# Optimization experiments

Hardware: AMD Instinct MI355X
Metric: run time of the kernel (lower is better)

Reference implementation:

```python
import jax, jax.numpy as jnp
import numpy as np

B, NPG, DEG = 128, 400, 16
N, E = B * NPG, B * NPG * DEG
E_PER = E // B
K1, K2, K3 = 360, 324, 292  # ceil(0.9*400), ceil(0.9*360), ceil(0.9*324)
EPS = 1e-5


def setup_inputs() -> dict:
    key = jax.random.key(0)
    ks = jax.random.split(key, 48)
    # edges constrained within each graph (contiguous equal-size graphs)
    g = jnp.repeat(jnp.arange(B, dtype=jnp.int32), E_PER)
    src = jax.random.randint(ks[0], (E,), 0, NPG, dtype=jnp.int32) + g * NPG
    dst = jax.random.randint(ks[1], (E,), 0, NPG, dtype=jnp.int32) + g * NPG
    inp = {
        'x': jax.random.normal(ks[2], (N, 64), dtype=jnp.float32),
        'edge_index': jnp.stack([src, dst]),
        'batch': jnp.repeat(jnp.arange(B, dtype=jnp.int32), NPG),
    }
    def glorot(k, a, b):
        lim = float(np.sqrt(6.0 / (a + b)))
        return jax.random.uniform(k, (a, b), minval=-lim, maxval=lim, dtype=jnp.float32)
    conv_dims = [(64, 32), (32, 64), (64, 128), (128, 128)]
    for i, (a, b) in enumerate(conv_dims, 1):
        inp[f'W{i}'] = glorot(ks[2 + i], a, b)
        inp[f'b{i}'] = jnp.zeros((b,), jnp.float32)
    for i, d in zip((1, 2, 3), (32, 64, 128)):
        inp[f'p{i}'] = jax.random.uniform(ks[8 + i], (d,), minval=-1.0, maxval=1.0, dtype=jnp.float32) / float(np.sqrt(d))
    lin_dims = [(128, 64), (64, 64), (64, 32), (32, 16), (16, 1)]
    for i, (a, b) in enumerate(lin_dims, 1):
        inp[f'Lw{i}'] = glorot(ks[12 + i], a, b)
        inp[f'Lb{i}'] = jnp.zeros((b,), jnp.float32)
    for i, d in enumerate((64, 64, 32, 16), 1):
        inp[f'g{i}'] = jnp.ones((d,), jnp.float32)
        inp[f'be{i}'] = jnp.zeros((d,), jnp.float32)
    return inp


def _gcn(x, src, dst, emask, nmask, W, b):
    h = x @ W
    deg = nmask + jax.ops.segment_sum(emask, dst, num_segments=N)
    dinv = jnp.where(deg > 0, jax.lax.rsqrt(deg), 0.0)
    norm = dinv[src] * dinv[dst] * emask
    agg = jax.ops.segment_sum(h[src] * norm[:, None], dst, num_segments=N)
    agg = agg + h * (dinv * dinv * nmask)[:, None]  # self-loop term
    return (agg + b) * nmask[:, None]


def _topk_pool(x, nmask, p, k):
    # PyG TopKPooling: score = x.p/||p||, keep top-k per graph, x *= tanh(score)
    score = (x @ p) / jnp.linalg.norm(p)
    sel = jnp.where(nmask > 0, score, -jnp.inf).reshape(B, NPG)
    _, idx = jax.lax.top_k(sel, k)
    gidx = (idx + (jnp.arange(B) * NPG)[:, None]).reshape(-1)
    new_mask = jnp.zeros((N,), x.dtype).at[gidx].set(1.0)
    return x * (jnp.tanh(score) * new_mask)[:, None], new_mask


def reference(x, edge_index, batch, W1, b1, p1, W2, b2, p2, W3, b3, p3, W4, b4,
              Lw1, Lb1, Lw2, Lb2, Lw3, Lb3, Lw4, Lb4, Lw5, Lb5,
              g1, be1, g2, be2, g3, be3, g4, be4):
    src, dst = edge_index[0], edge_index[1]
    nmask = jnp.ones((N,), jnp.float32)
    emask = jnp.ones((E,), jnp.float32)
    x = jax.nn.relu(_gcn(x, src, dst, emask, nmask, W1, b1))
    x, nmask = _topk_pool(x, nmask, p1, K1)
    emask = emask * nmask[src] * nmask[dst]
    x = jax.nn.relu(_gcn(x, src, dst, emask, nmask, W2, b2))
    x, nmask = _topk_pool(x, nmask, p2, K2)
    emask = emask * nmask[src] * nmask[dst]
    x = jax.nn.relu(_gcn(x, src, dst, emask, nmask, W3, b3))
    x, nmask = _topk_pool(x, nmask, p3, K3)
    emask = emask * nmask[src] * nmask[dst]
    x = jax.nn.relu(_gcn(x, src, dst, emask, nmask, W4, b4))
    h = x.reshape(B, NPG, -1).max(axis=1)
    def lin_bn(h, W, bb, ga, be):
        h = h @ W + bb
        m = h.mean(0)
        v = h.var(0)  # biased, matches BatchNorm1d training normalization
        return jax.nn.relu(ga * (h - m) / jnp.sqrt(v + EPS) + be)
    h = lin_bn(h, Lw1, Lb1, g1, be1)
    h = lin_bn(h, Lw2, Lb2, g2, be2)
    h = lin_bn(h, Lw3, Lb3, g3, be3)
    h = lin_bn(h, Lw4, Lb4, g4, be4)
    return h @ Lw5 + Lb5
```

## Files before the change

kernel.cpp:

```cpp
#include <hip/hip_runtime.h>
#include <math.h>

#define NNODES 51200
#define BGRAPHS 128
#define NPG 400
#define NEDGES 819200
#define EPG 6400
#define SLP 7680

__global__ __launch_bounds__(512) void csr_build_kernel(
    const int* __restrict__ src, const int* __restrict__ dst,
    unsigned short* __restrict__ slg, int* __restrict__ gsg, int* __restrict__ gcg,
    float* __restrict__ nmask, float* __restrict__ dinv, float* __restrict__ sc,
    float* __restrict__ hp) {
    __shared__ int deg[NPG];
    __shared__ int incl[512];
    __shared__ int gs[NPG];
    __shared__ int cur[NPG];
    const int g = blockIdx.x, t = threadIdx.x;
    for (int i = t; i < NPG; i += 512) deg[i] = 0;
    if (t < 128) hp[g * 128 + t] = 0.0f;
    __syncthreads();
    for (int e = t; e < EPG; e += 512)
        atomicAdd(&deg[dst[g * EPG + e] - g * NPG], 1);
    __syncthreads();
    const int d = (t < NPG) ? deg[t] : 0;
    const int p = (d + 3) >> 2;
    incl[t] = p;
    __syncthreads();
    for (int off = 1; off < 512; off <<= 1) {
        int add = (t >= off) ? incl[t - off] : 0;
        __syncthreads();
        incl[t] += add;
        __syncthreads();
    }
    if (t < NPG) {
        const int gstart = incl[t] - p;
        gs[t] = gstart;
        gsg[g * NPG + t] = gstart;
        gcg[g * NPG + t] = p;
        cur[t] = gstart * 4;
        nmask[g * NPG + t] = 1.0f;
        const float dv = rsqrtf(1.0f + (float)d);
        dinv[g * NPG + t] = dv;
        sc[g * NPG + t] = dv;
    }
    __syncthreads();
    for (int e = t; e < EPG; e += 512) {
        int dl = dst[g * EPG + e] - g * NPG;
        int pos = atomicAdd(&cur[dl], 1);
        slg[g * SLP + pos] = (unsigned short)(src[g * EPG + e] - g * NPG);
    }
    __syncthreads();
    if (t < NPG) {
        const int end = (gs[t] + p) * 4;
        for (int i = cur[t]; i < end; i++) slg[g * SLP + i] = (unsigned short)NPG;
    }
}

template<int IN, int OUT, int MODE>
__global__ __launch_bounds__(256) void gemm_kernel(
    const float* __restrict__ X, const float* __restrict__ W,
    const float* __restrict__ bias, const float* __restrict__ nmask,
    float* __restrict__ H, const float* __restrict__ p,
    float* __restrict__ score, float* __restrict__ hp) {
    __shared__ __align__(16) float sX[64 * IN];
    __shared__ unsigned smax[256];
    const int row0 = blockIdx.x * 64;
    const int t = threadIdx.x;
    for (int i = t; i < 64 * IN / 4; i += 256)
        reinterpret_cast<float4*>(sX)[i] =
            reinterpret_cast<const float4*>(X + (size_t)row0 * IN)[i];
    if (MODE == 3) smax[t] = 0u;
    __syncthreads();
    constexpr int CG  = OUT / 4;
    constexpr int RG  = 256 / CG;
    constexpr int RPT = 64 / RG;
    const int c0 = (t % CG) * 4;
    const int r0 = (t / CG) * RPT;
    float acc[RPT][4];
#pragma unroll
    for (int r = 0; r < RPT; r++)
#pragma unroll
        for (int j = 0; j < 4; j++) acc[r][j] = 0.0f;
    for (int k4 = 0; k4 < IN / 4; k4++) {
        const float4 w0 = *reinterpret_cast<const float4*>(&W[(k4 * 4 + 0) * OUT + c0]);
        const float4 w1 = *reinterpret_cast<const float4*>(&W[(k4 * 4 + 1) * OUT + c0]);
        const float4 w2 = *reinterpret_cast<const float4*>(&W[(k4 * 4 + 2) * OUT + c0]);
        const float4 w3 = *reinterpret_cast<const float4*>(&W[(k4 * 4 + 3) * OUT + c0]);
#pragma unroll
        for (int r = 0; r < RPT; r++) {
            const float4 xv = *reinterpret_cast<const float4*>(&sX[(r0 + r) * IN + k4 * 4]);
            acc[r][0] += xv.x * w0.x + xv.y * w1.x + xv.z * w2.x + xv.w * w3.x;
            acc[r][1] += xv.x * w0.y + xv.y * w1.y + xv.z * w2.y + xv.w * w3.y;
            acc[r][2] += xv.x * w0.z + xv.y * w1.z + xv.z * w2.z + xv.w * w3.z;
            acc[r][3] += xv.x * w0.w + xv.y * w1.w + xv.z * w2.w + xv.w * w3.w;
        }
    }
    const int graph0 = row0 / 400;
    const int bnd = (graph0 + 1) * 400;
    float ps[RPT];
#pragma unroll
    for (int r = 0; r < RPT; r++) {
        const int row = row0 + r0 + r;
        float4 v = make_float4(acc[r][0], acc[r][1], acc[r][2], acc[r][3]);
        if (MODE >= 2) {
            const float4 b4 = *reinterpret_cast<const float4*>(&bias[c0]);
            const float m = nmask[row];
            v.x = fmaxf(v.x + b4.x, 0.0f) * m;
            v.y = fmaxf(v.y + b4.y, 0.0f) * m;
            v.z = fmaxf(v.z + b4.z, 0.0f) * m;
            v.w = fmaxf(v.w + b4.w, 0.0f) * m;
        }
        if (MODE != 3) *reinterpret_cast<float4*>(&H[(size_t)row * OUT + c0]) = v;
        if (MODE == 2) {
            const float4 p4 = *reinterpret_cast<const float4*>(&p[c0]);
            ps[r] = v.x * p4.x + v.y * p4.y + v.z * p4.z + v.w * p4.w;
        }
        if (MODE == 3) {
            const int seg = (row >= bnd) ? 1 : 0;
            const float mx = fmaxf(fmaxf(v.x, v.y), fmaxf(v.z, v.w));
            atomicMax(&smax[seg * 128 + c0 + 0], __float_as_uint(v.x));
            atomicMax(&smax[seg * 128 + c0 + 1], __float_as_uint(v.y));
            atomicMax(&smax[seg * 128 + c0 + 2], __float_as_uint(v.z));
            atomicMax(&smax[seg * 128 + c0 + 3], __float_as_uint(v.w));
            (void)mx;
        }
    }
    if (MODE == 2) {
#pragma unroll
        for (int r = 0; r < RPT; r++) {
#pragma unroll
            for (int off = 1; off < CG; off <<= 1) ps[r] += __shfl_xor(ps[r], off);
        }
        if ((t % CG) == 0) {
#pragma unroll
            for (int r = 0; r < RPT; r++) score[row0 + r0 + r] = ps[r];
        }
    }
    if (MODE == 3) {
        __syncthreads();
        unsigned* hpu = reinterpret_cast<unsigned*>(hp);
        if (t < 128) atomicMax(&hpu[graph0 * 128 + t], smax[t]);
        const int graph1 = (row0 + 63) / 400;
        if (graph1 != graph0 && t < 128) atomicMax(&hpu[graph1 * 128 + t], smax[128 + t]);
    }
}

template<int OUT, int NCH, int NS, bool EPI, bool SCORE>
__global__ __launch_bounds__(512) void gcn_agg_kernel(
    const float* __restrict__ H, float* __restrict__ Y,
    const float* __restrict__ dinv, const float* __restrict__ sc,
    const float* __restrict__ bias, const float* __restrict__ p,
    float* __restrict__ score,
    const unsigned short* __restrict__ slg, const int* __restrict__ gsg,
    const int* __restrict__ gcg) {
    __shared__ __align__(16) float Hl[(NPG + 1) * 36];
    __shared__ float dinvl[NPG];
    __shared__ int gsl[NPG];
    __shared__ int gcl[NPG];
    __shared__ unsigned long long sl64[SLP / 4];
    const unsigned short* sl = reinterpret_cast<const unsigned short*>(sl64);
    const int b   = blockIdx.x;
    const int g   = b / (NCH * NS);
    const int rem = b % (NCH * NS);
    const int f0  = (rem / NS) * 32;
    const int n0  = (rem % NS) * (NPG / NS);
    const int t   = threadIdx.x;

    for (int i = t; i < NPG; i += 512) {
        dinvl[i] = dinv[g * NPG + i];
        gsl[i] = gsg[g * NPG + i];
        gcl[i] = gcg[g * NPG + i];
    }
    for (int i = t; i < SLP / 4; i += 512)
        sl64[i] = reinterpret_cast<const unsigned long long*>(slg + (size_t)g * SLP)[i];
    if (t < 36) Hl[NPG * 36 + t] = 0.0f;
    for (int i = t; i < NPG * 8; i += 512) {
        const int n = i >> 3, q = i & 7;
        const float s = sc[g * NPG + n];
        float4 v = *reinterpret_cast<const float4*>(&H[(size_t)(g * NPG + n) * OUT + f0 + q * 4]);
        v.x *= s; v.y *= s; v.z *= s; v.w *= s;
        *reinterpret_cast<float4*>(&Hl[n * 36 + q * 4]) = v;
    }
    __syncthreads();

    const int wave = t >> 6, lane = t & 63;
    const int sub = lane >> 3, f4 = lane & 7;
    constexpr int NPB = NPG / NS;
    for (int n = n0 + wave * 8 + sub; n < n0 + NPB; n += 64) {
        const float di = dinvl[n];
        if (di == 0.0f) continue;
        const int g0 = gsl[n], g1 = g0 + gcl[n];
        float4 acc = *reinterpret_cast<const float4*>(&Hl[n * 36 + f4 * 4]);
        for (int gg = g0; gg < g1; ++gg) {
            const unsigned long long q = *reinterpret_cast<const unsigned long long*>(&sl[gg * 4]);
            const int s0 = (int)(q & 0xFFFF), s1 = (int)((q >> 16) & 0xFFFF);
            const int s2 = (int)((q >> 32) & 0xFFFF), s3 = (int)(q >> 48);
            const float4 a = *reinterpret_cast<const float4*>(&Hl[s0 * 36 + f4 * 4]);
            const float4 bb = *reinterpret_cast<const float4*>(&Hl[s1 * 36 + f4 * 4]);
            const float4 c = *reinterpret_cast<const float4*>(&Hl[s2 * 36 + f4 * 4]);
            const float4 dd = *reinterpret_cast<const float4*>(&Hl[s3 * 36 + f4 * 4]);
            acc.x += (a.x + bb.x) + (c.x + dd.x);
            acc.y += (a.y + bb.y) + (c.y + dd.y);
            acc.z += (a.z + bb.z) + (c.z + dd.z);
            acc.w += (a.w + bb.w) + (c.w + dd.w);
        }
        acc.x *= di; acc.y *= di; acc.z *= di; acc.w *= di;
        if (EPI) {
            const float4 b4 = *reinterpret_cast<const float4*>(&bias[f0 + f4 * 4]);
            acc.x = fmaxf(acc.x + b4.x, 0.0f);
            acc.y = fmaxf(acc.y + b4.y, 0.0f);
            acc.z = fmaxf(acc.z + b4.z, 0.0f);
            acc.w = fmaxf(acc.w + b4.w, 0.0f);
        }
        *reinterpret_cast<float4*>(&Y[(size_t)(g * NPG + n) * OUT + f0 + f4 * 4]) = acc;
        if (SCORE) {
            const float4 p4 = *reinterpret_cast<const float4*>(&p[f4 * 4]);
            float part = acc.x * p4.x + acc.y * p4.y + acc.z * p4.z + acc.w * p4.w;
            part += __shfl_xor(part, 1);
            part += __shfl_xor(part, 2);
            part += __shfl_xor(part, 4);
            if (f4 == 0) score[g * NPG + n] = part;
        }
    }
}

template<int DIM>
__global__ __launch_bounds__(512) void topk_kernel(
    const float* __restrict__ score, float* __restrict__ nmask,
    float* __restrict__ dinv, float* __restrict__ sc,
    const float* __restrict__ p, int K,
    const unsigned short* __restrict__ slg, const int* __restrict__ gsg,
    const int* __restrict__ gcg) {
    __shared__ float sval[512];
    __shared__ int   sidx[512];
    __shared__ float sraw[NPG];
    __shared__ float nml[NPG + 1];
    __shared__ unsigned long long sl64[SLP / 4];
    __shared__ int gsl[NPG];
    __shared__ int gcl[NPG];
    __shared__ float spnorm;
    const unsigned short* sl = reinterpret_cast<const unsigned short*>(sl64);
    const int g = blockIdx.x;
    const int t = threadIdx.x;
    for (int i = t; i < SLP / 4; i += 512)
        sl64[i] = reinterpret_cast<const unsigned long long*>(slg + (size_t)g * SLP)[i];
    for (int i = t; i < NPG; i += 512) {
        gsl[i] = gsg[g * NPG + i];
        gcl[i] = gcg[g * NPG + i];
    }
    if (t == 0) {
        float s = 0.0f;
        for (int j = 0; j < DIM; j++) s += p[j] * p[j];
        spnorm = sqrtf(s);
    }
    __syncthreads();
    if (t < NPG) {
        const float raw = score[g * NPG + t];
        sraw[t] = raw;
        sval[t] = (nmask[g * NPG + t] > 0.0f) ? raw : -INFINITY;
        sidx[t] = t;
    } else {
        sval[t] = -INFINITY;
        sidx[t] = 0x7FFFFFFF;
    }
    __syncthreads();
    for (int kk = 2; kk <= 512; kk <<= 1) {
        for (int j = kk >> 1; j > 0; j >>= 1) {
            int l = t ^ j;
            if (l > t) {
                float va = sval[t], vb = sval[l];
                int   ia = sidx[t], ib = sidx[l];
                bool aFirst = (va > vb) || (va == vb && ia < ib);
                bool desc   = ((t & kk) == 0);
                if (desc != aFirst) {
                    sval[t] = vb; sval[l] = va;
                    sidx[t] = ib; sidx[l] = ia;
                }
            }
            __syncthreads();
        }
    }
    if (t <= NPG) nml[t] = 0.0f;
    __syncthreads();
    if (t < K) nml[sidx[t]] = 1.0f;
    __syncthreads();
    if (t < NPG) nmask[g * NPG + t] = nml[t];
    for (int n = t; n < NPG; n += 512) {
        float dv = 0.0f;
        if (nml[n] > 0.0f) {
            float d = 1.0f;
            const int g0 = gsl[n], g1 = g0 + gcl[n];
            for (int gg = g0; gg < g1; ++gg) {
                const unsigned long long q = *reinterpret_cast<const unsigned long long*>(&sl[gg * 4]);
                d += nml[(int)(q & 0xFFFF)] + nml[(int)((q >> 16) & 0xFFFF)] +
                     nml[(int)((q >> 32) & 0xFFFF)] + nml[(int)(q >> 48)];
            }
            dv = rsqrtf(d);
        }
        dinv[g * NPG + n] = dv;
        sc[g * NPG + n] = (nml[n] > 0.0f) ? tanhf(sraw[n] / spnorm) * dv : 0.0f;
    }
}

template<int IN, int OUT>
__global__ __launch_bounds__(128) void head_layer_kernel(
    const float* __restrict__ A, const float* __restrict__ W,
    const float* __restrict__ b, const float* __restrict__ ga,
    const float* __restrict__ be, float* __restrict__ Y) {
    __shared__ float Al[128 * (IN + 1)];
    __shared__ float red[4];
    const int c = blockIdx.x, t = threadIdx.x;
    for (int i = t; i < 128 * IN; i += 128)
        Al[(i / IN) * (IN + 1) + (i % IN)] = A[i];
    __syncthreads();
    float acc = b[c];
#pragma unroll
    for (int j = 0; j < IN; j++) acc += Al[t * (IN + 1) + j] * W[j * OUT + c];
    float s1 = acc, s2 = acc * acc;
    for (int o = 32; o > 0; o >>= 1) {
        s1 += __shfl_down(s1, o, 64);
        s2 += __shfl_down(s2, o, 64);
    }
    if ((t & 63) == 0) { red[t >> 6] = s1; red[2 + (t >> 6)] = s2; }
    __syncthreads();
    const float S1 = red[0] + red[1], S2 = red[2] + red[3];
    const float m = S1 * (1.0f / 128.0f);
    const float var = S2 * (1.0f / 128.0f) - m * m;
    float val = ga[c] * (acc - m) * rsqrtf(var + 1e-5f) + be[c];
    Y[t * OUT + c] = fmaxf(val, 0.0f);
}

__global__ __launch_bounds__(128) void head_final_kernel(
    const float* __restrict__ A, const float* __restrict__ w,
    const float* __restrict__ b, float* __restrict__ out) {
    const int t = threadIdx.x;
    float acc = b[0];
#pragma unroll
    for (int j = 0; j < 16; j++) acc += A[t * 16 + j] * w[j];
    out[t] = acc;
}

extern "C" void kernel_launch(void* const* d_in, const int* in_sizes, int n_in,
                              void* d_out, int out_size, void* d_ws, size_t ws_size,
                              hipStream_t stream) {
    (void)in_sizes; (void)n_in; (void)out_size; (void)ws_size;
    const float* x   = (const float*)d_in[0];
    const int*   ei  = (const int*)d_in[1];
    const float* W1  = (const float*)d_in[3];  const float* b1  = (const float*)d_in[4];
    const float* W2  = (const float*)d_in[5];  const float* b2  = (const float*)d_in[6];
    const float* W3  = (const float*)d_in[7];  const float* b3  = (const float*)d_in[8];
    const float* W4  = (const float*)d_in[9];  const float* b4  = (const float*)d_in[10];
    const float* p1  = (const float*)d_in[11];
    const float* p2  = (const float*)d_in[12];
    const float* p3  = (const float*)d_in[13];
    const float* Lw1 = (const float*)d_in[14]; const float* Lb1 = (const float*)d_in[15];
    const float* Lw2 = (const float*)d_in[16]; const float* Lb2 = (const float*)d_in[17];
    const float* Lw3 = (const float*)d_in[18]; const float* Lb3 = (const float*)d_in[19];
    const float* Lw4 = (const float*)d_in[20]; const float* Lb4 = (const float*)d_in[21];
    const float* Lw5 = (const float*)d_in[22]; const float* Lb5 = (const float*)d_in[23];
    const float* g1  = (const float*)d_in[24]; const float* be1 = (const float*)d_in[25];
    const float* g2  = (const float*)d_in[26]; const float* be2 = (const float*)d_in[27];
    const float* g3  = (const float*)d_in[28]; const float* be3 = (const float*)d_in[29];
    const float* g4  = (const float*)d_in[30]; const float* be4 = (const float*)d_in[31];

    const int* src = ei;
    const int* dst = ei + NEDGES;

    float* ws    = (float*)d_ws;
    float* hb    = ws;
    float* x0    = hb + (size_t)NNODES * 128;
    float* x1    = x0 + (size_t)NNODES * 128;
    float* nmask = x1 + (size_t)NNODES * 128;
    float* dinv  = nmask + NNODES;
    float* sc    = dinv + NNODES;
    float* scoreb= sc + NNODES;
    float* hp    = scoreb + NNODES;
    float* a1    = hp + 128 * 128;
    float* a2    = a1 + 128 * 64;
    float* a3    = a2 + 128 * 64;
    float* a4    = a3 + 128 * 32;
    unsigned short* slg = (unsigned short*)(a4 + 128 * 16);
    int* gsg = (int*)(slg + (size_t)BGRAPHS * SLP);
    int* gcg = gsg + (size_t)BGRAPHS * NPG;

    csr_build_kernel<<<BGRAPHS, 512, 0, stream>>>(src, dst, slg, gsg, gcg, nmask, dinv, sc, hp);

    gemm_kernel<64, 32, 0><<<NNODES / 64, 256, 0, stream>>>(x, W1, nullptr, nullptr, hb, nullptr, nullptr, nullptr);
    gcn_agg_kernel<32, 1, 2, true, true><<<BGRAPHS * 2, 512, 0, stream>>>(hb, x0, dinv, sc, b1, p1, scoreb, slg, gsg, gcg);
    topk_kernel<32><<<BGRAPHS, 512, 0, stream>>>(scoreb, nmask, dinv, sc, p1, 360, slg, gsg, gcg);

    gcn_agg_kernel<32, 1, 2, false, false><<<BGRAPHS * 2, 512, 0, stream>>>(x0, hb, dinv, sc, nullptr, nullptr, nullptr, slg, gsg, gcg);
    gemm_kernel<32, 64, 2><<<NNODES / 64, 256, 0, stream>>>(hb, W2, b2, nmask, x1, p2, scoreb, nullptr);
    topk_kernel<64><<<BGRAPHS, 512, 0, stream>>>(scoreb, nmask, dinv, sc, p2, 324, slg, gsg, gcg);

    gcn_agg_kernel<64, 2, 2, false, false><<<BGRAPHS * 4, 512, 0, stream>>>(x1, hb, dinv, sc, nullptr, nullptr, nullptr, slg, gsg, gcg);
    gemm_kernel<64, 128, 2><<<NNODES / 64, 256, 0, stream>>>(hb, W3, b3, nmask, x0, p3, scoreb, nullptr);
    topk_kernel<128><<<BGRAPHS, 512, 0, stream>>>(scoreb, nmask, dinv, sc, p3, 292, slg, gsg, gcg);

    gcn_agg_kernel<128, 4, 1, false, false><<<BGRAPHS * 4, 512, 0, stream>>>(x0, hb, dinv, sc, nullptr, nullptr, nullptr, slg, gsg, gcg);
    gemm_kernel<128, 128, 3><<<NNODES / 64, 256, 0, stream>>>(hb, W4, b4, nmask, x1, nullptr, nullptr, hp);

    head_layer_kernel<128, 64><<<64, 128, 0, stream>>>(hp, Lw1, Lb1, g1, be1, a1);
    head_layer_kernel<64, 64><<<64, 128, 0, stream>>>(a1, Lw2, Lb2, g2, be2, a2);
    head_layer_kernel<64, 32><<<32, 128, 0, stream>>>(a2, Lw3, Lb3, g3, be3, a3);
    head_layer_kernel<32, 16><<<16, 128, 0, stream>>>(a3, Lw4, Lb4, g4, be4, a4);
    head_final_kernel<<<1, 128, 0, stream>>>(a4, Lw5, Lb5, (float*)d_out);
}
```

Baseline: 209.5 us.

## Fuse MLP head into one kernel, shuffle-based bitonic topk, register max-pool

Replaces the five head kernels (four linear+batchnorm layers and the final linear) with a single 512-thread block that keeps activations and weights in shared memory, removing launch and global round-trip overhead. The topk bitonic sort now keeps values in registers and uses wave shuffles for strides below 64, needing shared memory and barriers only for larger strides. The final GEMM's max pool reduces each thread's rows in registers before issuing the shared atomics. The segment choice is now made once per thread, which risks misattributing rows if a thread's rows straddle a graph boundary.

```diff
diff --git a/kernel.cpp b/kernel.cpp
--- a/kernel.cpp
+++ b/kernel.cpp
@@ -100,6 +100,7 @@
     const int graph0 = row0 / 400;
     const int bnd = (graph0 + 1) * 400;
     float ps[RPT];
+    float cmax[4] = {0.f, 0.f, 0.f, 0.f};
 #pragma unroll
     for (int r = 0; r < RPT; r++) {
         const int row = row0 + r0 + r;
@@ -118,13 +119,10 @@
             ps[r] = v.x * p4.x + v.y * p4.y + v.z * p4.z + v.w * p4.w;
         }
         if (MODE == 3) {
-            const int seg = (row >= bnd) ? 1 : 0;
-            const float mx = fmaxf(fmaxf(v.x, v.y), fmaxf(v.z, v.w));
-            atomicMax(&smax[seg * 128 + c0 + 0], __float_as_uint(v.x));
-            atomicMax(&smax[seg * 128 + c0 + 1], __float_as_uint(v.y));
-            atomicMax(&smax[seg * 128 + c0 + 2], __float_as_uint(v.z));
-            atomicMax(&smax[seg * 128 + c0 + 3], __float_as_uint(v.w));
-            (void)mx;
+            cmax[0] = fmaxf(cmax[0], v.x);
+            cmax[1] = fmaxf(cmax[1], v.y);
+            cmax[2] = fmaxf(cmax[2], v.z);
+            cmax[3] = fmaxf(cmax[3], v.w);
         }
     }
     if (MODE == 2) {
@@ -139,6 +137,11 @@
         }
     }
     if (MODE == 3) {
+        const int seg = ((row0 + r0) >= bnd) ? 1 : 0;
+        atomicMax(&smax[seg * 128 + c0 + 0], __float_as_uint(cmax[0]));
+        atomicMax(&smax[seg * 128 + c0 + 1], __float_as_uint(cmax[1]));
+        atomicMax(&smax[seg * 128 + c0 + 2], __float_as_uint(cmax[2]));
+        atomicMax(&smax[seg * 128 + c0 + 3], __float_as_uint(cmax[3]));
         __syncthreads();
         unsigned* hpu = reinterpret_cast<unsigned*>(hp);
         if (t < 128) atomicMax(&hpu[graph0 * 128 + t], smax[t]);
@@ -255,36 +258,36 @@
         for (int j = 0; j < DIM; j++) s += p[j] * p[j];
         spnorm = sqrtf(s);
     }
-    __syncthreads();
+    float v = -INFINITY;
+    int ix = t;
     if (t < NPG) {
         const float raw = score[g * NPG + t];
         sraw[t] = raw;
-        sval[t] = (nmask[g * NPG + t] > 0.0f) ? raw : -INFINITY;
-        sidx[t] = t;
-    } else {
-        sval[t] = -INFINITY;
-        sidx[t] = 0x7FFFFFFF;
+        v = (nmask[g * NPG + t] > 0.0f) ? raw : -INFINITY;
     }
     __syncthreads();
     for (int kk = 2; kk <= 512; kk <<= 1) {
         for (int j = kk >> 1; j > 0; j >>= 1) {
-            int l = t ^ j;
-            if (l > t) {
-                float va = sval[t], vb = sval[l];
-                int   ia = sidx[t], ib = sidx[l];
-                bool aFirst = (va > vb) || (va == vb && ia < ib);
-                bool desc   = ((t & kk) == 0);
-                if (desc != aFirst) {
-                    sval[t] = vb; sval[l] = va;
-                    sidx[t] = ib; sidx[l] = ia;
-                }
+            float vb; int ib;
+            if (j >= 64) {
+                sval[t] = v; sidx[t] = ix;
+                __syncthreads();
+                vb = sval[t ^ j]; ib = sidx[t ^ j];
+                __syncthreads();
+            } else {
+                vb = __shfl_xor(v, j, 64);
+                ib = __shfl_xor(ix, j, 64);
             }
-            __syncthreads();
+            const bool ownFirst = (v > vb) || (v == vb && ix < ib);
+            const bool lower = (t & j) == 0;
+            const bool desc = (t & kk) == 0;
+            const bool keepOwn = lower ? (desc == ownFirst) : (desc != ownFirst);
+            if (!keepOwn) { v = vb; ix = ib; }
         }
     }
     if (t <= NPG) nml[t] = 0.0f;
     __syncthreads();
-    if (t < K) nml[sidx[t]] = 1.0f;
+    if (t < K) nml[ix] = 1.0f;
     __syncthreads();
     if (t < NPG) nmask[g * NPG + t] = nml[t];
     for (int n = t; n < NPG; n += 512) {
@@ -304,42 +307,93 @@
     }
 }
 
-template<int IN, int OUT>
-__global__ __launch_bounds__(128) void head_layer_kernel(
-    const float* __restrict__ A, const float* __restrict__ W,
-    const float* __restrict__ b, const float* __restrict__ ga,
-    const float* __restrict__ be, float* __restrict__ Y) {
-    __shared__ float Al[128 * (IN + 1)];
-    __shared__ float red[4];
-    const int c = blockIdx.x, t = threadIdx.x;
-    for (int i = t; i < 128 * IN; i += 128)
-        Al[(i / IN) * (IN + 1) + (i % IN)] = A[i];
-    __syncthreads();
-    float acc = b[c];
-#pragma unroll
-    for (int j = 0; j < IN; j++) acc += Al[t * (IN + 1) + j] * W[j * OUT + c];
-    float s1 = acc, s2 = acc * acc;
-    for (int o = 32; o > 0; o >>= 1) {
-        s1 += __shfl_down(s1, o, 64);
-        s2 += __shfl_down(s2, o, 64);
-    }
-    if ((t & 63) == 0) { red[t >> 6] = s1; red[2 + (t >> 6)] = s2; }
-    __syncthreads();
-    const float S1 = red[0] + red[1], S2 = red[2] + red[3];
-    const float m = S1 * (1.0f / 128.0f);
-    const float var = S2 * (1.0f / 128.0f) - m * m;
-    float val = ga[c] * (acc - m) * rsqrtf(var + 1e-5f) + be[c];
-    Y[t * OUT + c] = fmaxf(val, 0.0f);
-}
-
-__global__ __launch_bounds__(128) void head_final_kernel(
-    const float* __restrict__ A, const float* __restrict__ w,
-    const float* __restrict__ b, float* __restrict__ out) {
+template<int IN, int OUT, int SA, int SO>
+__device__ __forceinline__ void hlayer(float* A, float* Bf, float* Wl, float* smv,
+                                       const float* __restrict__ W,
+                                       const float* __restrict__ b,
+                                       const float* __restrict__ ga,
+                                       const float* __restrict__ be, int t) {
+    for (int i = t; i < IN * OUT / 4; i += 512)
+        reinterpret_cast<float4*>(Wl)[i] = reinterpret_cast<const float4*>(W)[i];
+    __syncthreads();
+    constexpr int RGS = 512 / OUT;
+    constexpr int RPT = 128 / RGS;
+    constexpr int SB  = OUT + 1;
+    const int c = t % OUT, rg = t / OUT;
+    const int rbase = rg * RPT;
+    float acc[RPT];
+#pragma unroll
+    for (int k = 0; k < RPT; k++) acc[k] = 0.0f;
+    for (int j4 = 0; j4 < IN / 4; j4++) {
+        const float w0 = Wl[(j4 * 4 + 0) * OUT + c];
+        const float w1 = Wl[(j4 * 4 + 1) * OUT + c];
+        const float w2 = Wl[(j4 * 4 + 2) * OUT + c];
+        const float w3 = Wl[(j4 * 4 + 3) * OUT + c];
+#pragma unroll
+        for (int k = 0; k < RPT; k++) {
+            const float4 a = *reinterpret_cast<const float4*>(&A[(rbase + k) * SA + j4 * 4]);
+            acc[k] += a.x * w0 + a.y * w1 + a.z * w2 + a.w * w3;
+        }
+    }
+    const float bias = b[c];
+#pragma unroll
+    for (int k = 0; k < RPT; k++) Bf[(rbase + k) * SB + c] = acc[k] + bias;
+    __syncthreads();
+    if (t < OUT) {
+        float s1 = 0.0f, s2 = 0.0f;
+        for (int r = 0; r < 128; r++) {
+            const float vv = Bf[r * SB + t];
+            s1 += vv; s2 += vv * vv;
+        }
+        const float m = s1 * (1.0f / 128.0f);
+        smv[t] = m;
+        smv[64 + t] = s2 * (1.0f / 128.0f) - m * m;
+    }
+    __syncthreads();
+    const float m = smv[c];
+    const float scn = ga[c] * rsqrtf(smv[64 + c] + 1e-5f);
+    const float bb = be[c];
+#pragma unroll
+    for (int k = 0; k < RPT; k++) {
+        const float val = (acc[k] + bias - m) * scn + bb;
+        A[(rbase + k) * SO + c] = fmaxf(val, 0.0f);
+    }
+    __syncthreads();
+}
+
+__global__ __launch_bounds__(512) void head_kernel(
+    const float* __restrict__ HP,
+    const float* __restrict__ Lw1, const float* __restrict__ Lb1,
+    const float* __restrict__ Lw2, const float* __restrict__ Lb2,
+    const float* __restrict__ Lw3, const float* __restrict__ Lb3,
+    const float* __restrict__ Lw4, const float* __restrict__ Lb4,
+    const float* __restrict__ Lw5, const float* __restrict__ Lb5,
+    const float* __restrict__ g1, const float* __restrict__ be1,
+    const float* __restrict__ g2, const float* __restrict__ be2,
+    const float* __restrict__ g3, const float* __restrict__ be3,
+    const float* __restrict__ g4, const float* __restrict__ be4,
+    float* __restrict__ out) {
+    __shared__ __align__(16) float A[128 * 132];
+    __shared__ float Bf[128 * 65];
+    __shared__ __align__(16) float Wl[128 * 64];
+    __shared__ float smv[128];
     const int t = threadIdx.x;
-    float acc = b[0];
-#pragma unroll
-    for (int j = 0; j < 16; j++) acc += A[t * 16 + j] * w[j];
-    out[t] = acc;
+    for (int i = t; i < 128 * 32; i += 512) {
+        const int r = i >> 5, q = i & 31;
+        reinterpret_cast<float4*>(&A[r * 132])[q] =
+            reinterpret_cast<const float4*>(&HP[r * 128])[q];
+    }
+    __syncthreads();
+    hlayer<128, 64, 132, 68>(A, Bf, Wl, smv, Lw1, Lb1, g1, be1, t);
+    hlayer<64, 64, 68, 68>(A, Bf, Wl, smv, Lw2, Lb2, g2, be2, t);
+    hlayer<64, 32, 68, 36>(A, Bf, Wl, smv, Lw3, Lb3, g3, be3, t);
+    hlayer<32, 16, 36, 20>(A, Bf, Wl, smv, Lw4, Lb4, g4, be4, t);
+    if (t < 128) {
+        float acc = Lb5[0];
+#pragma unroll
+        for (int j = 0; j < 16; j++) acc += A[t * 20 + j] * Lw5[j];
+        out[t] = acc;
+    }
 }
 
 extern "C" void kernel_launch(void* const* d_in, const int* in_sizes, int n_in,
@@ -377,11 +431,7 @@
     float* sc    = dinv + NNODES;
     float* scoreb= sc + NNODES;
     float* hp    = scoreb + NNODES;
-    float* a1    = hp + 128 * 128;
-    float* a2    = a1 + 128 * 64;
-    float* a3    = a2 + 128 * 64;
-    float* a4    = a3 + 128 * 32;
-    unsigned short* slg = (unsigned short*)(a4 + 128 * 16);
+    unsigned short* slg = (unsigned short*)(hp + 128 * 128);
     int* gsg = (int*)(slg + (size_t)BGRAPHS * SLP);
     int* gcg = gsg + (size_t)BGRAPHS * NPG;
 
@@ -402,9 +452,7 @@
     gcn_agg_kernel<128, 4, 1, false, false><<<BGRAPHS * 4, 512, 0, stream>>>(x0, hb, dinv, sc, nullptr, nullptr, nullptr, slg, gsg, gcg);
     gemm_kernel<128, 128, 3><<<NNODES / 64, 256, 0, stream>>>(hb, W4, b4, nmask, x1, nullptr, nullptr, hp);
 
-    head_layer_kernel<128, 64><<<64, 128, 0, stream>>>(hp, Lw1, Lb1, g1, be1, a1);
-    head_layer_kernel<64, 64><<<64, 128, 0, stream>>>(a1, Lw2, Lb2, g2, be2, a2);
-    head_layer_kernel<64, 32><<<32, 128, 0, stream>>>(a2, Lw3, Lb3, g3, be3, a3);
-    head_layer_kernel<32, 16><<<16, 128, 0, stream>>>(a3, Lw4, Lb4, g4, be4, a4);
-    head_final_kernel<<<1, 128, 0, stream>>>(a4, Lw5, Lb5, (float*)d_out);
-}
+    head_kernel<<<1, 512, 0, stream>>>(hp,
+        Lw1, Lb1, Lw2, Lb2, Lw3, Lb3, Lw4, Lb4, Lw5, Lb5,
+        g1, be1, g2, be2, g3, be3, g4, be4, (float*)d_out);
+}
```

Measured after the change: 214.8 us. 2.5% more time.
